# Optimization experiments

Hardware: AMD Instinct MI355X
Metric: run time of the kernel (lower is better)

## Reference

```python
import jax, jax.numpy as jnp
import numpy as np

G = 8      # deform_groups
KK = 9     # 3x3 kernel positions


def conv2d(x, w, b, pad):
    out = jax.lax.conv_general_dilated(
        x, w, window_strides=(1, 1), padding=[(pad, pad), (pad, pad)],
        dimension_numbers=('NCHW', 'OIHW', 'NCHW'))
    return out + b[None, :, None, None]


def deform_conv(x, offset, w):
    # x: [B,C,H,W], offset: [B, G*2*KK, H, W] (mmcv layout: per group, per kernel pos k: (dy, dx)),
    # w: [Cout, C, 3, 3]. Zero padding outside image (mmcv DeformConv2d semantics), pad=1, stride=1.
    B, C, H, W = x.shape
    Cg = C // G
    off = offset.reshape(B, G, KK, 2, H, W)
    dy, dx = off[:, :, :, 0], off[:, :, :, 1]            # [B,G,KK,H,W]
    ky = jnp.repeat(jnp.arange(3) - 1, 3)                # kernel row offsets, (kh,kw) order
    kx = jnp.tile(jnp.arange(3) - 1, 3)
    sy = dy + jnp.arange(H)[None, :, None] + ky[:, None, None]   # [B,G,KK,H,W]
    sx = dx + jnp.arange(W)[None, None, :] + kx[:, None, None]
    y0 = jnp.floor(sy); x0 = jnp.floor(sx)
    wy = sy - y0; wx = sx - x0
    y0i = y0.astype(jnp.int32); x0i = x0.astype(jnp.int32)
    xg = x.reshape(B, G, Cg, H * W)

    def gather(yi, xi):
        valid = ((yi >= 0) & (yi < H) & (xi >= 0) & (xi < W)).astype(x.dtype)
        idx = jnp.clip(yi, 0, H - 1) * W + jnp.clip(xi, 0, W - 1)
        vals = jnp.take_along_axis(xg, idx.reshape(B, G, 1, KK * H * W), axis=3)
        return vals.reshape(B, G, Cg, KK, H, W) * valid[:, :, None]

    v00 = gather(y0i, x0i)
    v01 = gather(y0i, x0i + 1)
    v10 = gather(y0i + 1, x0i)
    v11 = gather(y0i + 1, x0i + 1)
    wy_ = wy[:, :, None]; wx_ = wx[:, :, None]           # [B,G,1,KK,H,W]
    samp = (v00 * (1 - wy_) * (1 - wx_) + v01 * (1 - wy_) * wx_
            + v10 * wy_ * (1 - wx_) + v11 * wy_ * wx_)   # [B,G,Cg,KK,H,W]
    wr = w.reshape(w.shape[0], G, Cg, KK)
    return jnp.einsum('ogck,bgckhw->bohw', wr, samp)


def reference(x, w_off1, b_off1, w_off2, b_off2, w_align1, w_alignf):
    B, T, C, H, W = x.shape
    # AvgPool3d kernel/stride [1,2,2]: spatial 2x2 mean per frame
    x2 = x.reshape(B, T, C, H // 2, 2, W // 2, 2).mean(axis=(4, 6))
    tc = T // 2
    fc1 = x[:, tc]
    fc2 = x2[:, tc]
    outs = []
    for i in range(T):
        if i == tc:
            outs.append(fc1)
            continue
        fn2 = x2[:, i]
        off2 = conv2d(jnp.concatenate([fn2, fc2], axis=1), w_off2, b_off2, pad=1)
        # bilinear upsample x2, align_corners=False (half-pixel, matches jax.image.resize)
        off2_us = jax.image.resize(off2, (B, off2.shape[1], H, W), method='bilinear') * 2.0
        fn1 = x[:, i]
        z1 = deform_conv(fn1, off2_us, w_align1)
        off1 = conv2d(jnp.concatenate([z1, fc1], axis=1), w_off1, b_off1, pad=2) + off2_us
        outs.append(deform_conv(fn1, off1, w_alignf))
    return jnp.stack(outs, axis=1)


def setup_inputs() -> dict:
    key = jax.random.key(0)
    ks = jax.random.split(key, 8)
    B, T, C, H, W = 2, 5, 64, 128, 128
    offC = G * 2 * KK  # 144
    return {
        'x': jax.random.normal(ks[0], (B, T, C, H, W), dtype=jnp.float32),
        # offset predictor weights kept small so sampled offsets are modest/realistic
        'w_off1': jax.random.normal(ks[1], (offC, 2 * C, 5, 5), dtype=jnp.float32) * 0.005,
        'b_off1': jnp.zeros((offC,), dtype=jnp.float32),
        'w_off2': jax.random.normal(ks[2], (offC, 2 * C, 3, 3), dtype=jnp.float32) * 0.005,
        'b_off2': jnp.zeros((offC,), dtype=jnp.float32),
        'w_align1': jax.random.normal(ks[3], (C, C, 3, 3), dtype=jnp.float32) * 0.05,
        'w_alignf': jax.random.normal(ks[4], (C, C, 3, 3), dtype=jnp.float32) * 0.05,
    }
```

## Files before the change

### kernel.cpp

```cpp
#include <hip/hip_runtime.h>
#include <cstdint>

#define BB 2
#define TT 5
#define CC 64
#define HH 128
#define WW 128
#define GG 8
#define KKD 9
#define OFFC 144
#define H2 64
#define W2 64
#define TCF 2
#define HW (HH*WW)
#define HW2 (H2*W2)
#define PLANE1 278784
#define PLANE0 69696

typedef __attribute__((ext_vector_type(4))) short short4v;
typedef __attribute__((ext_vector_type(8))) short short8;
typedef __attribute__((ext_vector_type(4))) float floatx4;
typedef __attribute__((ext_vector_type(16))) float floatx16;

static __device__ __forceinline__ unsigned short f2bf(float f) {
    unsigned int u = __float_as_uint(f);
    unsigned int r = (u + 0x7fffu + ((u >> 16) & 1u)) >> 16;
    return (unsigned short)r;
}

typedef __attribute__((address_space(1))) const unsigned int g_u32;
typedef __attribute__((address_space(3))) unsigned int l_u32;
static __device__ __forceinline__ void async16(const short* g, short* l) {
    __builtin_amdgcn_global_load_lds((g_u32*)g, (l_u32*)l, 16, 0, 0);
}

__global__ void wswzD_k(const float* __restrict__ w, short* __restrict__ ws) {
    int idx = blockIdx.x * 256 + threadIdx.x;
    if (idx >= 36864) return;
    int j = idx & 7;
    int lane = (idx >> 3) & 63;
    int tile = (idx >> 9) & 1;
    int chunk = idx >> 10;
    int ck = chunk * 16 + (lane >> 5) * 8 + j;
    int oc = tile * 32 + (lane & 31);
    int cin = ck / 9;
    int kt = ck - cin * 9;
    ws[idx] = (short)f2bf(w[((size_t)oc * 64 + cin) * 9 + kt]);
}

template <int TAPS>
__global__ void wswz_k(const float* __restrict__ w, short* __restrict__ ws) {
    int idx = blockIdx.x * 256 + threadIdx.x;
    if (idx >= 8 * TAPS * 5 * 512) return;
    int jj = idx & 7;
    int lane = (idx >> 3) & 63;
    int rest = idx >> 9;
    int ocF = rest % 5;
    int ct = rest / 5;
    int tap = ct % TAPS;
    int chunk = ct / TAPS;
    int oc = ocF * 32 + (lane & 31);
    int cin = chunk * 16 + (lane >> 5) * 8 + jj;
    float v = 0.f;
    if (oc < OFFC) v = w[((size_t)oc * 128 + cin) * TAPS + tap];
    ws[idx] = (short)f2bf(v);
}

__global__ void avgpool_k(const float* __restrict__ x, short* __restrict__ x2T) {
    __shared__ float sL[64 * 17];
    const int h2 = blockIdx.x;
    const int chunk = blockIdx.y;
    const int img = blockIdx.z;
    const int tid = threadIdx.x;
    const float* base = x + ((size_t)img * 64 + chunk * 16) * HW + (size_t)(2 * h2) * WW;
#pragma unroll
    for (int it = 0; it < 4; ++it) {
        int e = it * 256 + tid;
        int cin = e >> 6, w2 = e & 63;
        const float* sp = base + (size_t)cin * HW + 2 * w2;
        sL[w2 * 17 + cin] = 0.25f * (sp[0] + sp[1] + sp[WW] + sp[WW + 1]);
    }
    __syncthreads();
    int w2 = tid >> 2, cg = tid & 3;
    short4v sv;
#pragma unroll
    for (int q = 0; q < 4; ++q) sv[q] = (short)f2bf(sL[w2 * 17 + cg * 4 + q]);
    *(short4v*)&x2T[((size_t)img * 4 + chunk) * PLANE0 +
                    ((size_t)(h2 + 1) * 66 + (w2 + 1)) * 16 + cg * 4] = sv;
}

__global__ void xtrans_k(const float* __restrict__ x, short* __restrict__ xT) {
    __shared__ float sL[128 * 17];
    const int row = blockIdx.x;
    const int chunk = blockIdx.y;
    const int b = blockIdx.z;
    const int tid = threadIdx.x;
    const float* base = x + ((size_t)(b * 5 + TCF) * 64 + chunk * 16) * HW + (size_t)row * WW;
#pragma unroll
    for (int it = 0; it < 8; ++it) {
        int e = it * 256 + tid;
        int cin = e >> 7, col = e & 127;
        sL[col * 17 + cin] = base[(size_t)cin * HW + col];
    }
    __syncthreads();
    int col = tid >> 1, half = tid & 1;
    short8 sv;
#pragma unroll
    for (int q = 0; q < 8; ++q) sv[q] = (short)f2bf(sL[col * 17 + half * 8 + q]);
    *(short8*)&xT[((size_t)b * 4 + chunk) * PLANE1 +
                  ((size_t)(row + 2) * 132 + (col + 2)) * 16 + half * 8] = sv;
}

__global__ void xgt_k(const float* __restrict__ x, float* __restrict__ xg) {
    __shared__ float sL[128 * 9];
    const int row = blockIdx.x;
    const int g = blockIdx.y;
    const int bj = blockIdx.z;
    const int b = bj >> 2;
    const int j = bj & 3;
    const int i = j + (j >= 2 ? 1 : 0);
    const int tid = threadIdx.x;
    const float* base = x + ((size_t)(b * TT + i) * CC + g * 8) * HW + (size_t)row * WW;
#pragma unroll
    for (int it = 0; it < 4; ++it) {
        int e = it * 256 + tid;
        int cin = e >> 7, col = e & 127;
        sL[col * 9 + cin] = base[(size_t)cin * HW + col];
    }
    __syncthreads();
    int col = tid >> 1, half = tid & 1;
    floatx4 v;
#pragma unroll
    for (int q = 0; q < 4; ++q) v[q] = sL[col * 9 + half * 4 + q];
    *(floatx4*)&xg[(((size_t)(bj * 8 + g) * HW + row * WW + col) << 3) + half * 4] = v;
}

static __device__ __forceinline__ void conv0_body(
    const short* __restrict__ srcAT,
    const short* __restrict__ wswz, const float* __restrict__ bias,
    float* __restrict__ out) {
    constexpr int KS = 3;
    constexpr int IM = 64;
    constexpr int PD = IM + KS - 1;
    constexpr int TAPS = KS * KS;
    constexpr int OROWS = 4;
    constexpr int SROWS = OROWS + KS - 1;
    constexpr int PLANE = PD * PD * 16;
    constexpr int SLAB16 = SROWS * PD * 2;
    constexpr int BUFSH = SROWS * PD * 16;

    extern __shared__ __align__(16) short stg[];

    const int bj = blockIdx.z;
    const int b = bj >> 2;
    const int j = bj & 3;
    const int i = j + (j >= 2 ? 1 : 0);
    const int y0 = blockIdx.x * OROWS;
    const int tid = threadIdx.x;
    const int wave = tid >> 6;
    const int lane = tid & 63;
    const int l31 = lane & 31;
    const int quad = lane >> 5;
    const int wrb = wave >> 1;
    const int wc0 = (wave & 1) * 32;

    const short* srcA = srcAT + (size_t)((b * 5 + i) * 4) * PLANE;
    const short* srcB = srcAT + (size_t)((b * 5 + TCF) * 4) * PLANE;

    floatx16 acc[5];
#pragma unroll
    for (int o = 0; o < 5; ++o)
#pragma unroll
        for (int g = 0; g < 16; ++g) acc[o][g] = 0.f;

    auto stage = [&](int c, int sIdx) {
        const short* plane = (c < 4) ? (srcA + (size_t)c * PLANE)
                                     : (srcB + (size_t)(c - 4) * PLANE);
        const short* srcRow = plane + (size_t)y0 * (PD * 16);
        short* dst = stg + (size_t)sIdx * BUFSH;
        for (int base = wave * 64; base < SLAB16; base += 512) {
            int b2 = min(base, SLAB16 - 64);
            async16(srcRow + (size_t)(b2 + lane) * 8, dst + (size_t)b2 * 8);
        }
    };

    stage(0, 0);
    for (int c = 0; c < 8; ++c) {
        __syncthreads();
        if (c < 7) stage(c + 1, (c + 1) & 1);
        const short* sbuf = stg + (size_t)(c & 1) * BUFSH;
        const short* wpc = wswz + (size_t)c * TAPS * 2560 + lane * 8;
#pragma unroll 5
        for (int tap = 0; tap < TAPS; ++tap) {
            const int ky = tap / KS, kx = tap - ky * KS;
            short8 wf[5];
            const short* wp = wpc + (size_t)tap * 2560;
#pragma unroll
            for (int o = 0; o < 5; ++o) wf[o] = *(const short8*)(wp + o * 512);
            short8 pf = *(const short8*)(sbuf +
                ((size_t)(wrb + ky) * PD + (wc0 + kx + l31)) * 16 + quad * 8);
#pragma unroll
            for (int o = 0; o < 5; ++o)
                acc[o] = __builtin_amdgcn_mfma_f32_32x32x16_bf16(wf[o], pf, acc[o], 0, 0, 0);
        }
    }

    const size_t imgBase = (size_t)bj * OFFC * (IM * IM);
    const size_t rowAddr = imgBase + (size_t)(y0 + wrb) * IM + wc0 + l31;
#pragma unroll
    for (int o = 0; o < 5; ++o) {
        const int rmax = (o == 4) ? 8 : 16;
#pragma unroll
        for (int r = 0; r < 16; ++r) {
            if (r >= rmax) break;
            int oc = o * 32 + (r & 3) + 8 * (r >> 2) + 4 * quad;
            float v = acc[o][r] + bias[oc];
            out[rowAddr + (size_t)oc * (IM * IM)] = v;
        }
    }
}

__global__ __launch_bounds__(512) void convmf0_k(
    const short* __restrict__ srcAT,
    const short* __restrict__ wswz, const float* __restrict__ bias,
    float* __restrict__ out) {
    conv0_body(srcAT, wswz, bias, out);
}

__global__ __launch_bounds__(512) void convmf1_k(
    const short* __restrict__ srcAT, const short* __restrict__ srcBT,
    const short* __restrict__ wswz, const float* __restrict__ bias,
    const float* __restrict__ addend, float* __restrict__ out) {
    constexpr int KS = 5;
    constexpr int IM = 128;
    constexpr int PD = IM + KS - 1;
    constexpr int OROWS = 2;
    constexpr int SROWS = OROWS + KS - 1;
    constexpr int PLANE = PD * PD * 16;
    constexpr int SLAB16 = SROWS * PD * 2;
    constexpr int BUFSH = SROWS * PD * 16;
    constexpr int WP = 3 * 2560;

    extern __shared__ __align__(16) short lds[];
    short* pbuf = lds;
    short* wbuf = lds + 2 * BUFSH;

    const int bj = blockIdx.z;
    const int b = bj >> 2;
    const int y0 = blockIdx.x * OROWS;
    const int tid = threadIdx.x;
    const int wave = tid >> 6;
    const int lane = tid & 63;
    const int l31 = lane & 31;
    const int quad = lane >> 5;
    const int wrb = wave >> 2;
    const int wc0 = (wave & 3) * 32;

    const short* srcA = srcAT + (size_t)(bj * 4) * PLANE;
    const short* srcB = srcBT + (size_t)(b * 4) * PLANE;

    floatx16 acc[5];
#pragma unroll
    for (int o = 0; o < 5; ++o)
#pragma unroll
        for (int g = 0; g < 16; ++g) acc[o][g] = 0.f;

    auto stageP = [&](int c, int sIdx) {
        const short* plane = (c < 4) ? (srcA + (size_t)c * PLANE)
                                     : (srcB + (size_t)(c - 4) * PLANE);
        const short* srcRow = plane + (size_t)y0 * (PD * 16);
        short* dst = pbuf + (size_t)sIdx * BUFSH;
        for (int base = wave * 64; base < SLAB16; base += 512) {
            int b2 = min(base, SLAB16 - 64);
            async16(srcRow + (size_t)(b2 + lane) * 8, dst + (size_t)b2 * 8);
        }
    };
    auto stageW = [&](int c, int qoff, int qn, int sIdx) {
        const short* src = wswz + (size_t)c * 64000 + (size_t)qoff * 2560;
        short* dst = wbuf + (size_t)sIdx * WP;
        const int n16 = qn * 320;
        for (int base = wave * 64; base < n16; base += 512) {
            int b2 = min(base, n16 - 64);
            async16(src + (size_t)(b2 + lane) * 8, dst + (size_t)b2 * 8);
        }
    };

    constexpr int NP = 9;
    constexpr int QOFF[NP] = {0, 3, 6, 9, 12, 15, 18, 21, 24};
    constexpr int QN[NP] = {3, 3, 3, 3, 3, 3, 3, 3, 1};

    stageP(0, 0);
    stageW(0, 0, 3, 0);
    for (int c = 0; c < 8; ++c) {
#pragma unroll
        for (int q = 0; q < NP; ++q) {
            __syncthreads();
            const int pb = (c + q) & 1;
            if (!(c == 7 && q == NP - 1)) {
                const int nc = (q == NP - 1) ? c + 1 : c;
                const int nq = (q == NP - 1) ? 0 : q + 1;
                stageW(nc, QOFF[nq], QN[nq], pb ^ 1);
            }
            if (q == 0 && c < 7) stageP(c + 1, (c + 1) & 1);
            const short* sbuf = pbuf + (size_t)(c & 1) * BUFSH;
            const short* wb = wbuf + (size_t)pb * WP + lane * 8;
#pragma unroll
            for (int t = 0; t < QN[q]; ++t) {
                const int tap = QOFF[q] + t;
                const int ky = tap / KS, kx = tap - ky * KS;
                short8 wf[5];
#pragma unroll
                for (int o = 0; o < 5; ++o)
                    wf[o] = *(const short8*)(wb + (t * 5 + o) * 512);
                short8 pf = *(const short8*)(sbuf +
                    ((size_t)(wrb + ky) * PD + (wc0 + kx + l31)) * 16 + quad * 8);
#pragma unroll
                for (int o = 0; o < 5; ++o)
                    acc[o] = __builtin_amdgcn_mfma_f32_32x32x16_bf16(wf[o], pf,
                                                                     acc[o], 0, 0, 0);
            }
        }
    }

    const size_t imgBase = (size_t)bj * OFFC * (IM * IM);
    const size_t rowAddr = imgBase + (size_t)(y0 + wrb) * IM + wc0 + l31;
#pragma unroll
    for (int o = 0; o < 5; ++o) {
        const int rmax = (o == 4) ? 8 : 16;
#pragma unroll
        for (int r = 0; r < 16; ++r) {
            if (r >= rmax) break;
            int oc = o * 32 + (r & 3) + 8 * (r >> 2) + 4 * quad;
            float v = acc[o][r] + bias[oc];
            size_t a = rowAddr + (size_t)oc * (IM * IM);
            out[a] = v + addend[a];
        }
    }
}

__global__ void upsample_k(const float* __restrict__ off2, float* __restrict__ off2u) {
    int idx = blockIdx.x * 256 + threadIdx.x;
    int ox = idx & 127;
    int oy = (idx >> 7) & 127;
    int p = idx >> 14;
    const float* sp = off2 + (size_t)p * HW2;
    float sy = 0.5f * oy - 0.25f;
    float sx = 0.5f * ox - 0.25f;
    float y0f = floorf(sy), x0f = floorf(sx);
    int y0 = (int)y0f, x0 = (int)x0f;
    float fy = sy - y0f, fx = sx - x0f;
    int y0c = max(y0, 0), y1c = min(y0 + 1, 63);
    int x0c = max(x0, 0), x1c = min(x0 + 1, 63);
    float v00 = sp[y0c * 64 + x0c], v01 = sp[y0c * 64 + x1c];
    float v10 = sp[y1c * 64 + x0c], v11 = sp[y1c * 64 + x1c];
    float v = v00 * (1.f - fy) * (1.f - fx) + v01 * (1.f - fy) * fx +
              v10 * fy * (1.f - fx) + v11 * fy * fx;
    off2u[idx] = 2.0f * v;
}

#define SROW 584
__global__ __launch_bounds__(256)
__attribute__((amdgpu_waves_per_eu(4, 4))) void dconv_k(
    const float* __restrict__ xg,
    const float* __restrict__ off,
    const short* __restrict__ wsw,
    float* __restrict__ out, short* __restrict__ z1T, int outMode) {
    const int bj = blockIdx.x;
    const int b = bj >> 2;
    const int j = bj & 3;
    const int i = j + (j >= 2 ? 1 : 0);
    const int seg = blockIdx.y;
    const int y = seg >> 2;
    const int x0 = (seg & 3) << 5;
    const int tid = threadIdx.x;

    __shared__ short sS[32 * SROW];
    float* Pbuf = (float*)sS;

    const float* offp = off + (size_t)bj * OFFC * HW + y * WW + x0;

    {
        const int g = tid >> 5;
        const int px = tid & 31;
        short* srow = sS + px * SROW + g * 72;
        const float* xgp = xg + ((size_t)(bj * 8 + g)) * ((size_t)HW * 8);
        const float* offg = offp + (size_t)(g * 18) * HW + px;
#pragma unroll 1
        for (int kg = 0; kg < 3; ++kg) {
            const int kyy = kg - 1;
            const float fyrow = (float)(y + kyy);
#pragma unroll
            for (int kk = 0; kk < 3; ++kk) {
                const int k = kg * 3 + kk;
                float dy = offg[(size_t)(k * 2) * HW];
                float dx = offg[(size_t)(k * 2 + 1) * HW];
                const int kxx = kk - 1;
                float sy = fyrow + dy;
                float sx = (float)(x0 + px + kxx) + dx;
                float y0f = floorf(sy), x0f = floorf(sx);
                int iy = (int)y0f, ix = (int)x0f;
                float wy = sy - y0f, wx = sx - x0f;
                bool yv0 = (iy >= 0) & (iy < HH);
                bool yv1 = (iy + 1 >= 0) & (iy + 1 < HH);
                bool xv0 = (ix >= 0) & (ix < WW);
                bool xv1 = (ix + 1 >= 0) & (ix + 1 < WW);
                float w00 = (yv0 && xv0) ? (1.f - wy) * (1.f - wx) : 0.f;
                float w01 = (yv0 && xv1) ? (1.f - wy) * wx : 0.f;
                float w10 = (yv1 && xv0) ? wy * (1.f - wx) : 0.f;
                float w11 = (yv1 && xv1) ? wy * wx : 0.f;
                int iy0 = min(max(iy, 0), HH - 1);
                int iy1 = min(max(iy + 1, 0), HH - 1);
                int ix0 = min(max(ix, 0), WW - 1);
                int ix1 = min(max(ix + 1, 0), WW - 1);
                const float* p00 = xgp + ((size_t)(iy0 * WW + ix0) << 3);
                const float* p01 = xgp + ((size_t)(iy0 * WW + ix1) << 3);
                const float* p10 = xgp + ((size_t)(iy1 * WW + ix0) << 3);
                const float* p11 = xgp + ((size_t)(iy1 * WW + ix1) << 3);
                floatx4 a00 = *(const floatx4*)p00, b00 = *(const floatx4*)(p00 + 4);
                floatx4 a01 = *(const floatx4*)p01, b01 = *(const floatx4*)(p01 + 4);
                floatx4 a10 = *(const floatx4*)p10, b10 = *(const floatx4*)(p10 + 4);
                floatx4 a11 = *(const floatx4*)p11, b11 = *(const floatx4*)(p11 + 4);
#pragma unroll
                for (int c = 0; c < 4; ++c) {
                    float v = a00[c] * w00 + a01[c] * w01 + a10[c] * w10 + a11[c] * w11;
                    srow[c * 9 + k] = (short)f2bf(v);
                    float v2 = b00[c] * w00 + b01[c] * w01 + b10[c] * w10 + b11[c] * w11;
                    srow[(c + 4) * 9 + k] = (short)f2bf(v2);
                }
            }
        }
    }
    __syncthreads();

    const int wv = tid >> 6;
    const int lane = tid & 63;
    const int tile = wv >> 1;
    const int kw = wv & 1;
    floatx16 acc;
#pragma unroll
    for (int g = 0; g < 16; ++g) acc[g] = 0.f;

    const short* aBase = sS + (lane & 31) * SROW + (lane >> 5) * 8;
    const short* bBase = wsw + ((size_t)tile * 64 + lane) * 8;
    for (int chunk = kw * 18; chunk < kw * 18 + 18; ++chunk) {
        short8 af = *(const short8*)(aBase + chunk * 16);
        short8 bf = *(const short8*)(bBase + (size_t)chunk * 1024);
        acc = __builtin_amdgcn_mfma_f32_32x32x16_bf16(af, bf, acc, 0, 0, 0);
    }

    __syncthreads();
    {
        const int n = lane & 31;
#pragma unroll
        for (int g = 0; g < 16; ++g) {
            int m = (g & 3) + 8 * (g >> 2) + 4 * (lane >> 5);
            Pbuf[wv * 1056 + m * 33 + n] = acc[g];
        }
    }
    __syncthreads();

    if (outMode == 0) {
        const int chunk = tid >> 6;
        const int px = (tid >> 1) & 31;
        const int half = tid & 1;
        const int t2 = chunk >> 1;
        const int n0 = (chunk & 1) * 16 + half * 8;
        short8 sv;
#pragma unroll
        for (int q = 0; q < 8; ++q) {
            float v = Pbuf[(t2 * 2) * 1056 + px * 33 + n0 + q] +
                      Pbuf[(t2 * 2 + 1) * 1056 + px * 33 + n0 + q];
            sv[q] = (short)f2bf(v);
        }
        *(short8*)&z1T[((size_t)bj * 4 + chunk) * PLANE1 +
                       ((size_t)(y + 2) * 132 + (x0 + 2 + px)) * 16 + half * 8] = sv;
    } else {
        const size_t planeBase = (size_t)(b * TT + i) * CC * HW;
        const size_t rowBase = planeBase + (size_t)y * WW + x0;
#pragma unroll
        for (int rep = 0; rep < 8; ++rep) {
            int elem = rep * 256 + tid;
            int oc = elem >> 5;
            int px = elem & 31;
            int t = oc >> 5;
            int n = oc & 31;
            float v = Pbuf[(t * 2) * 1056 + px * 33 + n] +
                      Pbuf[(t * 2 + 1) * 1056 + px * 33 + n];
            out[rowBase + (size_t)oc * HW + px] = v;
        }
    }
}

__global__ void copy_center_k(const float* __restrict__ x, float* __restrict__ out) {
    int idx = blockIdx.x * 256 + threadIdx.x;
    int b = idx >> 18;
    int rem = idx & 262143;
    size_t o = (((size_t)(b * TT + TCF) * CC * HW) >> 2) + rem;
    ((float4*)out)[o] = ((const float4*)x)[o];
}

extern "C" void kernel_launch(void* const* d_in, const int* in_sizes, int n_in,
                              void* d_out, int out_size, void* d_ws, size_t ws_size,
                              hipStream_t stream) {
    const float* x = (const float*)d_in[0];
    const float* w_off1 = (const float*)d_in[1];
    const float* b_off1 = (const float*)d_in[2];
    const float* w_off2 = (const float*)d_in[3];
    const float* b_off2 = (const float*)d_in[4];
    const float* w_align1 = (const float*)d_in[5];
    const float* w_alignf = (const float*)d_in[6];
    float* out = (float*)d_out;
    float* ws = (float*)d_ws;

    float* off2 = ws;
    float* off2u = ws + 4718592;
    float* off1 = ws + 23592960;
    short* z1T = (short*)(ws + 42467328);
    short* xT = (short*)(ws + 46927872);
    short* x2T = (short*)(ws + 48043008);
    short* wsD1 = (short*)(ws + 49436928);
    short* wsDf = (short*)(ws + 49455360);
    short* w2s = (short*)(ws + 49473792);
    short* w1s = (short*)(ws + 49565952);
    float* xg = ws + 49821952;

    hipMemsetAsync((void*)z1T, 0, 27878400, stream);

    wswzD_k<<<144, 256, 0, stream>>>(w_align1, wsD1);
    wswzD_k<<<144, 256, 0, stream>>>(w_alignf, wsDf);
    wswz_k<9><<<720, 256, 0, stream>>>(w_off2, w2s);
    wswz_k<25><<<2000, 256, 0, stream>>>(w_off1, w1s);

    avgpool_k<<<dim3(64, 4, 10), 256, 0, stream>>>(x, x2T);
    xtrans_k<<<dim3(128, 4, 2), 256, 0, stream>>>(x, xT);
    xgt_k<<<dim3(128, 8, 8), 256, 0, stream>>>(x, xg);

    convmf0_k<<<dim3(16, 1, 8), 512, 25344, stream>>>(x2T, w2s, b_off2, off2);
    upsample_k<<<73728, 256, 0, stream>>>(off2, off2u);
    dconv_k<<<dim3(8, 512), 256, 0, stream>>>(xg, off2u, wsD1, nullptr, z1T, 0);
    convmf1_k<<<dim3(64, 1, 8), 512, 81408, stream>>>(z1T, xT, w1s, b_off1,
                                                      off2u, off1);
    dconv_k<<<dim3(8, 512), 256, 0, stream>>>(xg, off1, wsDf, out, nullptr, 1);
    copy_center_k<<<2048, 256, 0, stream>>>(x, out);
}
```

Before: 477.4 us.

## Split 5x5 offset conv across output-channel groups with 2-wide pixel register tiles

The 5x5 offset-prediction MFMA conv is split over blockIdx.y into two output-channel halves (3 and 2 MFMA tiles of 32 channels). Each block now runs 4 waves, and each wave covers 64 pixels (two 32-column fragments) instead of 32. The weight staging is reindexed so each block loads only its own channel slice. This doubles the block count and lets each weight fragment feed two MFMAs, aiming for better occupancy and reuse. The cost is that every input slab is staged twice, once per channel split, and each wave holds more accumulator registers.

```diff
diff --git a/kernel.cpp b/kernel.cpp
--- a/kernel.cpp
+++ b/kernel.cpp
@@ -227,7 +227,8 @@
     conv0_body(srcAT, wswz, bias, out);
 }
 
-__global__ __launch_bounds__(512) void convmf1_k(
+template <int OCNT, int OBASE>
+static __device__ __forceinline__ void conv1_body(
     const short* __restrict__ srcAT, const short* __restrict__ srcBT,
     const short* __restrict__ wswz, const float* __restrict__ bias,
     const float* __restrict__ addend, float* __restrict__ out) {
@@ -239,7 +240,7 @@
     constexpr int PLANE = PD * PD * 16;
     constexpr int SLAB16 = SROWS * PD * 2;
     constexpr int BUFSH = SROWS * PD * 16;
-    constexpr int WP = 3 * 2560;
+    constexpr int WP = 3 * 3 * 512;
 
     extern __shared__ __align__(16) short lds[];
     short* pbuf = lds;
@@ -253,35 +254,41 @@
     const int lane = tid & 63;
     const int l31 = lane & 31;
     const int quad = lane >> 5;
-    const int wrb = wave >> 2;
-    const int wc0 = (wave & 3) * 32;
+    const int wrb = wave >> 1;
+    const int wc0 = (wave & 1) * 64;
 
     const short* srcA = srcAT + (size_t)(bj * 4) * PLANE;
     const short* srcB = srcBT + (size_t)(b * 4) * PLANE;
 
-    floatx16 acc[5];
-#pragma unroll
-    for (int o = 0; o < 5; ++o)
-#pragma unroll
-        for (int g = 0; g < 16; ++g) acc[o][g] = 0.f;
+    floatx16 acc[2][OCNT];
+#pragma unroll
+    for (int f = 0; f < 2; ++f)
+#pragma unroll
+        for (int o = 0; o < OCNT; ++o)
+#pragma unroll
+            for (int g = 0; g < 16; ++g) acc[f][o][g] = 0.f;
 
     auto stageP = [&](int c, int sIdx) {
         const short* plane = (c < 4) ? (srcA + (size_t)c * PLANE)
                                      : (srcB + (size_t)(c - 4) * PLANE);
         const short* srcRow = plane + (size_t)y0 * (PD * 16);
         short* dst = pbuf + (size_t)sIdx * BUFSH;
-        for (int base = wave * 64; base < SLAB16; base += 512) {
+        for (int base = wave * 64; base < SLAB16; base += 256) {
             int b2 = min(base, SLAB16 - 64);
             async16(srcRow + (size_t)(b2 + lane) * 8, dst + (size_t)b2 * 8);
         }
     };
     auto stageW = [&](int c, int qoff, int qn, int sIdx) {
-        const short* src = wswz + (size_t)c * 64000 + (size_t)qoff * 2560;
+        const short* src = wswz + (size_t)c * 64000;
         short* dst = wbuf + (size_t)sIdx * WP;
-        const int n16 = qn * 320;
-        for (int base = wave * 64; base < n16; base += 512) {
+        const int n16 = qn * OCNT * 64;
+        for (int base = wave * 64; base < n16; base += 256) {
             int b2 = min(base, n16 - 64);
-            async16(src + (size_t)(b2 + lane) * 8, dst + (size_t)b2 * 8);
+            int u = b2 + lane;
+            int tp = u / (OCNT * 64);
+            int wi = u - tp * (OCNT * 64);
+            async16(src + ((size_t)(qoff + tp) * 320 + OBASE * 64 + wi) * 8,
+                    dst + (size_t)u * 8);
         }
     };
 
@@ -308,34 +315,54 @@
             for (int t = 0; t < QN[q]; ++t) {
                 const int tap = QOFF[q] + t;
                 const int ky = tap / KS, kx = tap - ky * KS;
-                short8 wf[5];
-#pragma unroll
-                for (int o = 0; o < 5; ++o)
-                    wf[o] = *(const short8*)(wb + (t * 5 + o) * 512);
-                short8 pf = *(const short8*)(sbuf +
-                    ((size_t)(wrb + ky) * PD + (wc0 + kx + l31)) * 16 + quad * 8);
-#pragma unroll
-                for (int o = 0; o < 5; ++o)
-                    acc[o] = __builtin_amdgcn_mfma_f32_32x32x16_bf16(wf[o], pf,
-                                                                     acc[o], 0, 0, 0);
+                short8 wf[OCNT];
+#pragma unroll
+                for (int o = 0; o < OCNT; ++o)
+                    wf[o] = *(const short8*)(wb + (t * OCNT + o) * 512);
+                short8 pf[2];
+#pragma unroll
+                for (int f = 0; f < 2; ++f)
+                    pf[f] = *(const short8*)(sbuf +
+                        ((size_t)(wrb + ky) * PD + (wc0 + f * 32 + kx + l31)) * 16 +
+                        quad * 8);
+#pragma unroll
+                for (int o = 0; o < OCNT; ++o)
+#pragma unroll
+                    for (int f = 0; f < 2; ++f)
+                        acc[f][o] = __builtin_amdgcn_mfma_f32_32x32x16_bf16(
+                            wf[o], pf[f], acc[f][o], 0, 0, 0);
             }
         }
     }
 
     const size_t imgBase = (size_t)bj * OFFC * (IM * IM);
-    const size_t rowAddr = imgBase + (size_t)(y0 + wrb) * IM + wc0 + l31;
-#pragma unroll
-    for (int o = 0; o < 5; ++o) {
-        const int rmax = (o == 4) ? 8 : 16;
-#pragma unroll
-        for (int r = 0; r < 16; ++r) {
-            if (r >= rmax) break;
-            int oc = o * 32 + (r & 3) + 8 * (r >> 2) + 4 * quad;
-            float v = acc[o][r] + bias[oc];
-            size_t a = rowAddr + (size_t)oc * (IM * IM);
-            out[a] = v + addend[a];
-        }
-    }
+#pragma unroll
+    for (int f = 0; f < 2; ++f) {
+        const size_t rowAddr = imgBase + (size_t)(y0 + wrb) * IM + wc0 + f * 32 + l31;
+#pragma unroll
+        for (int o = 0; o < OCNT; ++o) {
+            const int rmax = ((OBASE + o) == 4) ? 8 : 16;
+#pragma unroll
+            for (int r = 0; r < 16; ++r) {
+                if (r >= rmax) break;
+                int oc = (OBASE + o) * 32 + (r & 3) + 8 * (r >> 2) + 4 * quad;
+                float v = acc[f][o][r] + bias[oc];
+                size_t a = rowAddr + (size_t)oc * (IM * IM);
+                out[a] = v + addend[a];
+            }
+        }
+    }
+}
+
+__global__ __launch_bounds__(256)
+__attribute__((amdgpu_waves_per_eu(2, 2))) void convmf1_k(
+    const short* __restrict__ srcAT, const short* __restrict__ srcBT,
+    const short* __restrict__ wswz, const float* __restrict__ bias,
+    const float* __restrict__ addend, float* __restrict__ out) {
+    if (blockIdx.y == 0)
+        conv1_body<3, 0>(srcAT, srcBT, wswz, bias, addend, out);
+    else
+        conv1_body<2, 3>(srcAT, srcBT, wswz, bias, addend, out);
 }
 
 __global__ void upsample_k(const float* __restrict__ off2, float* __restrict__ off2u) {
@@ -538,7 +565,7 @@
     convmf0_k<<<dim3(16, 1, 8), 512, 25344, stream>>>(x2T, w2s, b_off2, off2);
     upsample_k<<<73728, 256, 0, stream>>>(off2, off2u);
     dconv_k<<<dim3(8, 512), 256, 0, stream>>>(xg, off2u, wsD1, nullptr, z1T, 0);
-    convmf1_k<<<dim3(64, 1, 8), 512, 81408, stream>>>(z1T, xT, w1s, b_off1,
+    convmf1_k<<<dim3(64, 2, 8), 256, 69120, stream>>>(z1T, xT, w1s, b_off1,
                                                       off2u, off1);
     dconv_k<<<dim3(8, 512), 256, 0, stream>>>(xg, off1, wsDf, out, nullptr, 1);
     copy_center_k<<<2048, 256, 0, stream>>>(x, out);
```

Result: no change. 483.2 us (+1.2%).
